# Optimization experiments

Measured on AMD Instinct MI355X. Metric: run time of the kernel, lower is better.

## Reference

```python
import jax, jax.numpy as jnp
import numpy as np

NUM_HEADS = 16


def setup_inputs() -> dict:
    key = jax.random.key(0)
    ks = jax.random.split(key, 5)
    B, S, D = 2, 2048, 2048
    scale = 1.0 / np.sqrt(D)
    return {
        "x": jax.random.normal(ks[0], (B, S, D), dtype=jnp.float32),
        "W_q": jax.random.normal(ks[1], (D, D), dtype=jnp.float32) * scale,
        "W_k": jax.random.normal(ks[2], (D, D), dtype=jnp.float32) * scale,
        "W_v": jax.random.normal(ks[3], (D, D), dtype=jnp.float32) * scale,
        "W_o": jax.random.normal(ks[4], (D, D), dtype=jnp.float32) * scale,
        "b_o": jnp.zeros((D,), dtype=jnp.float32),
    }


def reference(x, W_q, W_k, W_v, W_o, b_o):
    B, S, D = x.shape
    H = NUM_HEADS
    hd = D // H
    # projections, split into heads: [B, H, S, hd]
    q = (x @ W_q).reshape(B, S, H, hd).transpose(0, 2, 1, 3)
    k = (x @ W_k).reshape(B, S, H, hd).transpose(0, 2, 1, 3)
    v = (x @ W_v).reshape(B, S, H, hd).transpose(0, 2, 1, 3)
    # causal attention with explicit score matrix [B, H, S, S]
    scores = jnp.einsum("bhqd,bhkd->bhqk", q, k) / jnp.sqrt(jnp.asarray(hd, x.dtype))
    causal = jnp.tril(jnp.ones((S, S), dtype=bool))  # True = keep
    scores = jnp.where(causal, scores, -jnp.inf)
    weights = jax.nn.softmax(scores, axis=-1)
    ctx = jnp.einsum("bhqk,bhkd->bhqd", weights, v)
    ctx = ctx.transpose(0, 2, 1, 3).reshape(B, S, D)
    return ctx @ W_o + b_o
```

## Files before the change

kernel.cpp:

```cpp
#include <hip/hip_runtime.h>
#include <stdint.h>

#define SQ_S 2048
#define DIM 2048
#define NH 16
#define HD 128
#define NB 2
#define NROWS (NB * SQ_S)
#define NQK (2 * DIM)

typedef __bf16 bf16x8 __attribute__((ext_vector_type(8)));
typedef float f32x4 __attribute__((ext_vector_type(4)));
typedef unsigned short u16;

__device__ __forceinline__ u16 f2bf(float f) {
    unsigned int u = __float_as_uint(f);
    u += 0x7FFF + ((u >> 16) & 1);
    return (u16)(u >> 16);
}

__device__ __forceinline__ void load_lds16(const u16* g, u16* lds) {
    __builtin_amdgcn_global_load_lds(
        (const __attribute__((address_space(1))) unsigned int*)(uintptr_t)g,
        (__attribute__((address_space(3))) unsigned int*)(unsigned int)(uintptr_t)lds,
        16, 0, 0);
}

__global__ __launch_bounds__(256) void cast_x_kernel(const float* __restrict__ in,
                                                     u16* __restrict__ out) {
    int i = (blockIdx.x * 256 + threadIdx.x) * 4;
    float4 v = *(const float4*)(in + i);
    ushort4 o;
    o.x = f2bf(v.x); o.y = f2bf(v.y); o.z = f2bf(v.z); o.w = f2bf(v.w);
    *(ushort4*)(out + i) = o;
}

__global__ __launch_bounds__(256) void transpose_w_kernel(
    const float* __restrict__ w0, const float* __restrict__ w1,
    const float* __restrict__ w2, const float* __restrict__ w3,
    u16* __restrict__ o0, u16* __restrict__ o1,
    u16* __restrict__ o2, u16* __restrict__ o3) {
    __shared__ u16 tile[64][65];
    int z = blockIdx.z;
    const float* in = z == 0 ? w0 : z == 1 ? w1 : z == 2 ? w2 : w3;
    u16* out = z == 0 ? o0 : z == 1 ? o1 : z == 2 ? o2 : o3;
    int r0 = blockIdx.y * 64, c0 = blockIdx.x * 64;
    int t = threadIdx.x;
#pragma unroll
    for (int i = 0; i < 16; ++i) {
        int idx = i * 256 + t;
        int r = idx >> 6, c = idx & 63;
        tile[r][c] = f2bf(in[(size_t)(r0 + r) * DIM + c0 + c]);
    }
    __syncthreads();
#pragma unroll
    for (int i = 0; i < 4; ++i) {
        int idx = i * 256 + t;
        int oc = idx >> 4;
        int r4 = (idx & 15) * 4;
        ushort4 v;
        v.x = tile[r4 + 0][oc]; v.y = tile[r4 + 1][oc];
        v.z = tile[r4 + 2][oc]; v.w = tile[r4 + 3][oc];
        *(ushort4*)(out + (size_t)(c0 + oc) * DIM + r0 + r4) = v;
    }
}

__global__ __launch_bounds__(256) void gemm_bt_bf16(const u16* __restrict__ A,
                                                    const u16* __restrict__ Bt,
                                                    u16* __restrict__ C,
                                                    int M, int N, int K) {
    __shared__ u16 As[128 * 64];
    __shared__ u16 Bs[128 * 64];
    int t = threadIdx.x;
    int w = t >> 6, l = t & 63;
    int wm = (w >> 1) * 64, wn = (w & 1) * 64;
    int lr = l & 15, q = l >> 4;
    int bm = blockIdx.y, bn = blockIdx.x;
    int st_gcol = (((t & 7) ^ ((t >> 3) & 7)) * 8);
    f32x4 acc[4][4] = {};

    for (int k0 = 0; k0 < K; k0 += 64) {
        __syncthreads();
#pragma unroll
        for (int c = 0; c < 4; ++c) {
            int e = c * 2048 + t * 8;
            int row = e >> 6;
            load_lds16(A + (size_t)(bm * 128 + row) * K + k0 + st_gcol, As + e);
        }
#pragma unroll
        for (int c = 0; c < 4; ++c) {
            int e = c * 2048 + t * 8;
            int row = e >> 6;
            load_lds16(Bt + (size_t)(bn * 128 + row) * K + k0 + st_gcol, Bs + e);
        }
        __syncthreads();
#pragma unroll
        for (int kk = 0; kk < 2; ++kk) {
            bf16x8 a[4], b[4];
#pragma unroll
            for (int mt = 0; mt < 4; ++mt)
                a[mt] = *(const bf16x8*)(As + (wm + mt * 16 + lr) * 64 +
                                         (((kk * 4 + q) ^ (lr & 7)) * 8));
#pragma unroll
            for (int nt = 0; nt < 4; ++nt)
                b[nt] = *(const bf16x8*)(Bs + (wn + nt * 16 + lr) * 64 +
                                         (((kk * 4 + q) ^ (lr & 7)) * 8));
#pragma unroll
            for (int mt = 0; mt < 4; ++mt)
#pragma unroll
                for (int nt = 0; nt < 4; ++nt)
                    acc[mt][nt] = __builtin_amdgcn_mfma_f32_16x16x32_bf16(a[mt], b[nt], acc[mt][nt], 0, 0, 0);
        }
    }
    int r0 = bm * 128 + wm, c0 = bn * 128 + wn;
#pragma unroll
    for (int mt = 0; mt < 4; ++mt)
#pragma unroll
        for (int nt = 0; nt < 4; ++nt)
#pragma unroll
            for (int r = 0; r < 4; ++r) {
                int row = r0 + mt * 16 + q * 4 + r;
                int col = c0 + nt * 16 + lr;
                C[(size_t)row * N + col] = f2bf(acc[mt][nt][r]);
            }
}

__global__ __launch_bounds__(256) void gemm_bt_f32b(const u16* __restrict__ A,
                                                    const u16* __restrict__ Bt,
                                                    float* __restrict__ C,
                                                    const float* __restrict__ bias,
                                                    int M, int N, int K) {
    __shared__ u16 As[128 * 64];
    __shared__ u16 Bs[128 * 64];
    int t = threadIdx.x;
    int w = t >> 6, l = t & 63;
    int wm = (w >> 1) * 64, wn = (w & 1) * 64;
    int lr = l & 15, q = l >> 4;
    int bm = blockIdx.y, bn = blockIdx.x;
    int st_gcol = (((t & 7) ^ ((t >> 3) & 7)) * 8);
    f32x4 acc[4][4] = {};

    for (int k0 = 0; k0 < K; k0 += 64) {
        __syncthreads();
#pragma unroll
        for (int c = 0; c < 4; ++c) {
            int e = c * 2048 + t * 8;
            int row = e >> 6;
            load_lds16(A + (size_t)(bm * 128 + row) * K + k0 + st_gcol, As + e);
        }
#pragma unroll
        for (int c = 0; c < 4; ++c) {
            int e = c * 2048 + t * 8;
            int row = e >> 6;
            load_lds16(Bt + (size_t)(bn * 128 + row) * K + k0 + st_gcol, Bs + e);
        }
        __syncthreads();
#pragma unroll
        for (int kk = 0; kk < 2; ++kk) {
            bf16x8 a[4], b[4];
#pragma unroll
            for (int mt = 0; mt < 4; ++mt)
                a[mt] = *(const bf16x8*)(As + (wm + mt * 16 + lr) * 64 +
                                         (((kk * 4 + q) ^ (lr & 7)) * 8));
#pragma unroll
            for (int nt = 0; nt < 4; ++nt)
                b[nt] = *(const bf16x8*)(Bs + (wn + nt * 16 + lr) * 64 +
                                         (((kk * 4 + q) ^ (lr & 7)) * 8));
#pragma unroll
            for (int mt = 0; mt < 4; ++mt)
#pragma unroll
                for (int nt = 0; nt < 4; ++nt)
                    acc[mt][nt] = __builtin_amdgcn_mfma_f32_16x16x32_bf16(a[mt], b[nt], acc[mt][nt], 0, 0, 0);
        }
    }
    int r0 = bm * 128 + wm, c0 = bn * 128 + wn;
#pragma unroll
    for (int mt = 0; mt < 4; ++mt)
#pragma unroll
        for (int nt = 0; nt < 4; ++nt)
#pragma unroll
            for (int r = 0; r < 4; ++r) {
                int row = r0 + mt * 16 + q * 4 + r;
                int col = c0 + nt * 16 + lr;
                C[(size_t)row * N + col] = acc[mt][nt][r] + bias[col];
            }
}

__global__ __launch_bounds__(256) void attn_kernel(const u16* __restrict__ Q,
                                                   const u16* __restrict__ K,
                                                   const u16* __restrict__ Vt,
                                                   u16* __restrict__ ctx,
                                                   int ldqk, int ldv) {
    __shared__ u16 Kl[2][64 * 128];
    __shared__ u16 Vl[2][128 * 64];
    __shared__ u16 Pl[4][16 * 64];
    int t = threadIdx.x;
    int w = t >> 6, l = t & 63;
    int lr = l & 15, q = l >> 4, lk = q * 8;
    int px = blockIdx.x, h = blockIdx.y, b = blockIdx.z;
    const float scale = 0.08838834764831845f;
    int stK_gcol = (((t & 15) ^ (t >> 4)) * 8);
    int stV_gcol = (((t & 7) ^ ((t >> 3) & 7)) * 8);
    const u16* Kbase = K + (size_t)b * SQ_S * ldqk + h * HD;
    const u16* Vbase = Vt + (size_t)(h * HD) * ldv + b * SQ_S;

#pragma unroll 1
    for (int pass = 0; pass < 2; ++pass) {
        int qt = pass == 0 ? px : 31 - px;
        int q0 = qt * 64;
        int njt = qt + 1;

        bf16x8 qf[4];
        {
            const u16* qp = Q + ((size_t)(b * SQ_S + q0 + w * 16 + lr)) * ldqk + h * HD;
#pragma unroll
            for (int kd = 0; kd < 4; ++kd)
                qf[kd] = *(const bf16x8*)(qp + kd * 32 + lk);
        }

        f32x4 o[8] = {};
        float l_r[4] = {0.f, 0.f, 0.f, 0.f};

        {
            int e = t * 8;
#pragma unroll
            for (int c = 0; c < 4; ++c) {
                int eK = c * 2048 + e;
                load_lds16(Kbase + (size_t)(eK >> 7) * ldqk + stK_gcol, Kl[0] + eK);
            }
#pragma unroll
            for (int c = 0; c < 4; ++c) {
                int eV = c * 2048 + e;
                load_lds16(Vbase + (size_t)(eV >> 6) * ldv + stV_gcol, Vl[0] + eV);
            }
        }

#pragma unroll 1
        for (int jt = 0; jt < njt; ++jt) {
            __syncthreads();
            if (jt + 1 < njt) {
                int j1 = (jt + 1) * 64;
                u16* Kd = Kl[(jt + 1) & 1];
                u16* Vd = Vl[(jt + 1) & 1];
                int e = t * 8;
#pragma unroll
                for (int c = 0; c < 4; ++c) {
                    int eK = c * 2048 + e;
                    load_lds16(Kbase + (size_t)(j1 + (eK >> 7)) * ldqk + stK_gcol, Kd + eK);
                }
#pragma unroll
                for (int c = 0; c < 4; ++c) {
                    int eV = c * 2048 + e;
                    load_lds16(Vbase + (size_t)(eV >> 6) * ldv + j1 + stV_gcol, Vd + eV);
                }
            }
            const u16* Kc = Kl[jt & 1];
            const u16* Vc = Vl[jt & 1];

            f32x4 s[4] = {};
#pragma unroll
            for (int kd = 0; kd < 4; ++kd) {
#pragma unroll
                for (int nt = 0; nt < 4; ++nt) {
                    bf16x8 kb = *(const bf16x8*)(Kc + (nt * 16 + lr) * 128 +
                                                 (((kd * 4 + q) ^ lr) * 8));
                    s[nt] = __builtin_amdgcn_mfma_f32_16x16x32_bf16(qf[kd], kb, s[nt], 0, 0, 0);
                }
            }
            bool diag = (jt == qt);
            float rs[4] = {0.f, 0.f, 0.f, 0.f};
            float pv[4][4];
#pragma unroll
            for (int nt = 0; nt < 4; ++nt)
#pragma unroll
                for (int r = 0; r < 4; ++r) {
                    float v = s[nt][r] * scale - 6.0f;
                    if (diag && (nt * 16 + lr > w * 16 + q * 4 + r)) v = -1.0e30f;
                    float pp = __expf(v);
                    pv[nt][r] = pp;
                    rs[r] += pp;
                }
#pragma unroll
            for (int d = 1; d < 16; d <<= 1)
#pragma unroll
                for (int r = 0; r < 4; ++r)
                    rs[r] += __shfl_xor(rs[r], d, 64);
#pragma unroll
            for (int r = 0; r < 4; ++r)
                l_r[r] += rs[r];
            u16* pw = Pl[w];
#pragma unroll
            for (int nt = 0; nt < 4; ++nt)
#pragma unroll
                for (int r = 0; r < 4; ++r) {
                    int prow = q * 4 + r;
                    int pcol = nt * 16 + lr;
                    pw[prow * 64 + (((pcol >> 3) ^ (prow & 7)) * 8) + (pcol & 7)] = f2bf(pv[nt][r]);
                }
            asm volatile("s_waitcnt lgkmcnt(0)" ::: "memory");
#pragma unroll
            for (int kj = 0; kj < 2; ++kj) {
                bf16x8 pa = *(const bf16x8*)(pw + lr * 64 + (((kj * 4 + q) ^ (lr & 7)) * 8));
#pragma unroll
                for (int nd = 0; nd < 8; ++nd) {
                    bf16x8 vb = *(const bf16x8*)(Vc + (nd * 16 + lr) * 64 +
                                                 (((kj * 4 + q) ^ (lr & 7)) * 8));
                    o[nd] = __builtin_amdgcn_mfma_f32_16x16x32_bf16(pa, vb, o[nd], 0, 0, 0);
                }
            }
        }
        float li[4];
#pragma unroll
        for (int r = 0; r < 4; ++r) li[r] = 1.f / l_r[r];
#pragma unroll
        for (int nd = 0; nd < 8; ++nd)
#pragma unroll
            for (int r = 0; r < 4; ++r) {
                int row = q0 + w * 16 + q * 4 + r;
                int col = h * HD + nd * 16 + lr;
                ctx[((size_t)(b * SQ_S + row)) * DIM + col] = f2bf(o[nd][r] * li[r]);
            }
        __syncthreads();
    }
}

extern "C" void kernel_launch(void* const* d_in, const int* in_sizes, int n_in,
                              void* d_out, int out_size, void* d_ws, size_t ws_size,
                              hipStream_t stream) {
    const float* x  = (const float*)d_in[0];
    const float* Wq = (const float*)d_in[1];
    const float* Wk = (const float*)d_in[2];
    const float* Wv = (const float*)d_in[3];
    const float* Wo = (const float*)d_in[4];
    const float* bo = (const float*)d_in[5];
    float* out = (float*)d_out;

    char* p = (char*)d_ws;
    const size_t SZ_ACT = (size_t)NROWS * DIM * 2;
    const size_t SZ_W   = (size_t)DIM * DIM * 2;
    u16* Xb   = (u16*)(p);
    u16* Wqkt = (u16*)(p + SZ_ACT);
    u16* Wvt  = (u16*)(p + SZ_ACT + 2 * SZ_W);
    u16* Wot  = (u16*)(p + SZ_ACT + 3 * SZ_W);
    u16* QK   = (u16*)(p + SZ_ACT + 4 * SZ_W);
    u16* Vt   = (u16*)(p + 3 * SZ_ACT + 4 * SZ_W);
    u16* Cx   = (u16*)(p + 4 * SZ_ACT + 4 * SZ_W);

    cast_x_kernel<<<(NROWS * DIM) / 1024, 256, 0, stream>>>(x, Xb);
    transpose_w_kernel<<<dim3(DIM / 64, DIM / 64, 4), 256, 0, stream>>>(
        Wq, Wk, Wv, Wo,
        Wqkt, Wqkt + (size_t)DIM * DIM, Wvt, Wot);
    gemm_bt_bf16<<<dim3(NQK / 128, NROWS / 128), 256, 0, stream>>>(Xb, Wqkt, QK, NROWS, NQK, DIM);
    gemm_bt_bf16<<<dim3(NROWS / 128, DIM / 128), 256, 0, stream>>>(Wvt, Xb, Vt, DIM, NROWS, DIM);
    attn_kernel<<<dim3(16, NH, NB), 256, 0, stream>>>(QK, QK + DIM, Vt, Cx, NQK, NROWS);
    gemm_bt_f32b<<<dim3(DIM / 128, NROWS / 128), 256, 0, stream>>>(Cx, Wot, out, bo, NROWS, DIM, DIM);
}
```

Before: 410.1 us.

## Fuse QKV projection, read K/V from global in attention, split-K output GEMM

```diff
diff --git a/kernel.cpp b/kernel.cpp
--- a/kernel.cpp
+++ b/kernel.cpp
@@ -7,7 +7,7 @@
 #define HD 128
 #define NB 2
 #define NROWS (NB * SQ_S)
-#define NQK (2 * DIM)
+#define NQKV (3 * DIM)
 
 typedef __bf16 bf16x8 __attribute__((ext_vector_type(8)));
 typedef float f32x4 __attribute__((ext_vector_type(4)));
@@ -65,6 +65,28 @@
     }
 }
 
+__global__ __launch_bounds__(256) void transpose_v_kernel(const u16* __restrict__ V,
+                                                          u16* __restrict__ Vt, int ldv) {
+    __shared__ u16 tile[64][72];
+    int s0 = blockIdx.x * 64, d0 = blockIdx.y * 64;
+    int bh = blockIdx.z;
+    int b = bh >> 4, h = bh & 15;
+    int t = threadIdx.x;
+#pragma unroll
+    for (int i = 0; i < 16; ++i) {
+        int idx = i * 256 + t;
+        int r = idx >> 6, c = idx & 63;
+        tile[r][c] = V[((size_t)(b * SQ_S + s0 + r)) * ldv + h * HD + d0 + c];
+    }
+    __syncthreads();
+#pragma unroll
+    for (int i = 0; i < 16; ++i) {
+        int idx = i * 256 + t;
+        int r = idx >> 6, c = idx & 63;
+        Vt[((size_t)(bh * HD + d0 + r)) * SQ_S + s0 + c] = tile[c][r];
+    }
+}
+
 __global__ __launch_bounds__(256) void gemm_bt_bf16(const u16* __restrict__ A,
                                                     const u16* __restrict__ Bt,
                                                     u16* __restrict__ C,
@@ -125,22 +147,23 @@
             }
 }
 
-__global__ __launch_bounds__(256) void gemm_bt_f32b(const u16* __restrict__ A,
+__global__ __launch_bounds__(256) void gemm_bt_f32s(const u16* __restrict__ A,
                                                     const u16* __restrict__ Bt,
-                                                    float* __restrict__ C,
-                                                    const float* __restrict__ bias,
-                                                    int M, int N, int K) {
+                                                    float* __restrict__ Cpart,
+                                                    int M, int N, int K, int Khalf) {
     __shared__ u16 As[128 * 64];
     __shared__ u16 Bs[128 * 64];
     int t = threadIdx.x;
     int w = t >> 6, l = t & 63;
     int wm = (w >> 1) * 64, wn = (w & 1) * 64;
     int lr = l & 15, q = l >> 4;
-    int bm = blockIdx.y, bn = blockIdx.x;
+    int bm = blockIdx.y, bn = blockIdx.x, z = blockIdx.z;
     int st_gcol = (((t & 7) ^ ((t >> 3) & 7)) * 8);
     f32x4 acc[4][4] = {};
-
-    for (int k0 = 0; k0 < K; k0 += 64) {
+    int kbeg = z * Khalf;
+
+    for (int kk0 = 0; kk0 < Khalf; kk0 += 64) {
+        int k0 = kbeg + kk0;
         __syncthreads();
 #pragma unroll
         for (int c = 0; c < 4; ++c) {
@@ -173,6 +196,7 @@
                     acc[mt][nt] = __builtin_amdgcn_mfma_f32_16x16x32_bf16(a[mt], b[nt], acc[mt][nt], 0, 0, 0);
         }
     }
+    float* Cp = Cpart + (size_t)z * M * N;
     int r0 = bm * 128 + wm, c0 = bn * 128 + wn;
 #pragma unroll
     for (int mt = 0; mt < 4; ++mt)
@@ -182,33 +206,42 @@
             for (int r = 0; r < 4; ++r) {
                 int row = r0 + mt * 16 + q * 4 + r;
                 int col = c0 + nt * 16 + lr;
-                C[(size_t)row * N + col] = acc[mt][nt][r] + bias[col];
-            }
+                Cp[(size_t)row * N + col] = acc[mt][nt][r];
+            }
+}
+
+__global__ __launch_bounds__(256) void reduce_bias_kernel(const float* __restrict__ P,
+                                                          float* __restrict__ out,
+                                                          const float* __restrict__ bias) {
+    int i = (blockIdx.x * 256 + threadIdx.x) * 4;
+    const size_t MN = (size_t)NROWS * DIM;
+    float4 a = *(const float4*)(P + i);
+    float4 c = *(const float4*)(P + MN + i);
+    float4 bb = *(const float4*)(bias + (i & (DIM - 1)));
+    float4 o;
+    o.x = a.x + c.x + bb.x; o.y = a.y + c.y + bb.y;
+    o.z = a.z + c.z + bb.z; o.w = a.w + c.w + bb.w;
+    *(float4*)(out + i) = o;
 }
 
 __global__ __launch_bounds__(256) void attn_kernel(const u16* __restrict__ Q,
                                                    const u16* __restrict__ K,
                                                    const u16* __restrict__ Vt,
-                                                   u16* __restrict__ ctx,
-                                                   int ldqk, int ldv) {
-    __shared__ u16 Kl[2][64 * 128];
-    __shared__ u16 Vl[2][128 * 64];
+                                                   u16* __restrict__ ctx, int ldqk) {
     __shared__ u16 Pl[4][16 * 64];
     int t = threadIdx.x;
     int w = t >> 6, l = t & 63;
     int lr = l & 15, q = l >> 4, lk = q * 8;
     int px = blockIdx.x, h = blockIdx.y, b = blockIdx.z;
     const float scale = 0.08838834764831845f;
-    int stK_gcol = (((t & 15) ^ (t >> 4)) * 8);
-    int stV_gcol = (((t & 7) ^ ((t >> 3) & 7)) * 8);
     const u16* Kbase = K + (size_t)b * SQ_S * ldqk + h * HD;
-    const u16* Vbase = Vt + (size_t)(h * HD) * ldv + b * SQ_S;
+    const u16* Vbase = Vt + ((size_t)(b * NH + h)) * HD * SQ_S;
+    u16* pw = Pl[w];
 
 #pragma unroll 1
     for (int pass = 0; pass < 2; ++pass) {
         int qt = pass == 0 ? px : 31 - px;
         int q0 = qt * 64;
-        int njt = qt + 1;
 
         bf16x8 qf[4];
         {
@@ -221,49 +254,16 @@
         f32x4 o[8] = {};
         float l_r[4] = {0.f, 0.f, 0.f, 0.f};
 
-        {
-            int e = t * 8;
-#pragma unroll
-            for (int c = 0; c < 4; ++c) {
-                int eK = c * 2048 + e;
-                load_lds16(Kbase + (size_t)(eK >> 7) * ldqk + stK_gcol, Kl[0] + eK);
-            }
-#pragma unroll
-            for (int c = 0; c < 4; ++c) {
-                int eV = c * 2048 + e;
-                load_lds16(Vbase + (size_t)(eV >> 6) * ldv + stV_gcol, Vl[0] + eV);
-            }
-        }
-
 #pragma unroll 1
-        for (int jt = 0; jt < njt; ++jt) {
-            __syncthreads();
-            if (jt + 1 < njt) {
-                int j1 = (jt + 1) * 64;
-                u16* Kd = Kl[(jt + 1) & 1];
-                u16* Vd = Vl[(jt + 1) & 1];
-                int e = t * 8;
-#pragma unroll
-                for (int c = 0; c < 4; ++c) {
-                    int eK = c * 2048 + e;
-                    load_lds16(Kbase + (size_t)(j1 + (eK >> 7)) * ldqk + stK_gcol, Kd + eK);
-                }
-#pragma unroll
-                for (int c = 0; c < 4; ++c) {
-                    int eV = c * 2048 + e;
-                    load_lds16(Vbase + (size_t)(eV >> 6) * ldv + j1 + stV_gcol, Vd + eV);
-                }
-            }
-            const u16* Kc = Kl[jt & 1];
-            const u16* Vc = Vl[jt & 1];
-
+        for (int jt = 0; jt <= qt; ++jt) {
+            int j0 = jt * 64;
             f32x4 s[4] = {};
 #pragma unroll
             for (int kd = 0; kd < 4; ++kd) {
 #pragma unroll
                 for (int nt = 0; nt < 4; ++nt) {
-                    bf16x8 kb = *(const bf16x8*)(Kc + (nt * 16 + lr) * 128 +
-                                                 (((kd * 4 + q) ^ lr) * 8));
+                    bf16x8 kb = *(const bf16x8*)(Kbase + (size_t)(j0 + nt * 16 + lr) * ldqk +
+                                                 kd * 32 + lk);
                     s[nt] = __builtin_amdgcn_mfma_f32_16x16x32_bf16(qf[kd], kb, s[nt], 0, 0, 0);
                 }
             }
@@ -288,7 +288,6 @@
 #pragma unroll
             for (int r = 0; r < 4; ++r)
                 l_r[r] += rs[r];
-            u16* pw = Pl[w];
 #pragma unroll
             for (int nt = 0; nt < 4; ++nt)
 #pragma unroll
@@ -303,8 +302,8 @@
                 bf16x8 pa = *(const bf16x8*)(pw + lr * 64 + (((kj * 4 + q) ^ (lr & 7)) * 8));
 #pragma unroll
                 for (int nd = 0; nd < 8; ++nd) {
-                    bf16x8 vb = *(const bf16x8*)(Vc + (nd * 16 + lr) * 64 +
-                                                 (((kj * 4 + q) ^ (lr & 7)) * 8));
+                    bf16x8 vb = *(const bf16x8*)(Vbase + (size_t)(nd * 16 + lr) * SQ_S +
+                                                 j0 + kj * 32 + lk);
                     o[nd] = __builtin_amdgcn_mfma_f32_16x16x32_bf16(pa, vb, o[nd], 0, 0, 0);
                 }
             }
@@ -320,7 +319,6 @@
                 int col = h * HD + nd * 16 + lr;
                 ctx[((size_t)(b * SQ_S + row)) * DIM + col] = f2bf(o[nd][r] * li[r]);
             }
-        __syncthreads();
     }
 }
 
@@ -336,22 +334,24 @@
     float* out = (float*)d_out;
 
     char* p = (char*)d_ws;
-    const size_t SZ_ACT = (size_t)NROWS * DIM * 2;
-    const size_t SZ_W   = (size_t)DIM * DIM * 2;
-    u16* Xb   = (u16*)(p);
-    u16* Wqkt = (u16*)(p + SZ_ACT);
-    u16* Wvt  = (u16*)(p + SZ_ACT + 2 * SZ_W);
-    u16* Wot  = (u16*)(p + SZ_ACT + 3 * SZ_W);
-    u16* QK   = (u16*)(p + SZ_ACT + 4 * SZ_W);
-    u16* Vt   = (u16*)(p + 3 * SZ_ACT + 4 * SZ_W);
-    u16* Cx   = (u16*)(p + 4 * SZ_ACT + 4 * SZ_W);
+    const size_t SZ_ACT  = (size_t)NROWS * DIM * 2;
+    const size_t SZ_W    = (size_t)DIM * DIM * 2;
+    const size_t SZ_QKV  = (size_t)NROWS * NQKV * 2;
+    u16*   Xb   = (u16*)(p);
+    u16*   Wqkv = (u16*)(p + SZ_ACT);
+    u16*   Wot  = (u16*)(p + SZ_ACT + 3 * SZ_W);
+    u16*   QKV  = (u16*)(p + SZ_ACT + 4 * SZ_W);
+    u16*   Vt   = (u16*)(p + SZ_ACT + 4 * SZ_W + SZ_QKV);
+    u16*   Cx   = (u16*)(p + 2 * SZ_ACT + 4 * SZ_W + SZ_QKV);
+    float* Pp   = (float*)(p + SZ_ACT + 4 * SZ_W);
 
     cast_x_kernel<<<(NROWS * DIM) / 1024, 256, 0, stream>>>(x, Xb);
     transpose_w_kernel<<<dim3(DIM / 64, DIM / 64, 4), 256, 0, stream>>>(
         Wq, Wk, Wv, Wo,
-        Wqkt, Wqkt + (size_t)DIM * DIM, Wvt, Wot);
-    gemm_bt_bf16<<<dim3(NQK / 128, NROWS / 128), 256, 0, stream>>>(Xb, Wqkt, QK, NROWS, NQK, DIM);
-    gemm_bt_bf16<<<dim3(NROWS / 128, DIM / 128), 256, 0, stream>>>(Wvt, Xb, Vt, DIM, NROWS, DIM);
-    attn_kernel<<<dim3(16, NH, NB), 256, 0, stream>>>(QK, QK + DIM, Vt, Cx, NQK, NROWS);
-    gemm_bt_f32b<<<dim3(DIM / 128, NROWS / 128), 256, 0, stream>>>(Cx, Wot, out, bo, NROWS, DIM, DIM);
-}
+        Wqkv, Wqkv + (size_t)DIM * DIM, Wqkv + 2 * (size_t)DIM * DIM, Wot);
+    gemm_bt_bf16<<<dim3(NQKV / 128, NROWS / 128), 256, 0, stream>>>(Xb, Wqkv, QKV, NROWS, NQKV, DIM);
+    transpose_v_kernel<<<dim3(SQ_S / 64, HD / 64, NB * NH), 256, 0, stream>>>(QKV + 2 * DIM, Vt, NQKV);
+    attn_kernel<<<dim3(16, NH, NB), 256, 0, stream>>>(QKV, QKV + DIM, Vt, Cx, NQKV);
+    gemm_bt_f32s<<<dim3(DIM / 128, NROWS / 128, 2), 256, 0, stream>>>(Cx, Wot, Pp, NROWS, DIM, DIM, DIM / 2);
+    reduce_bias_kernel<<<(NROWS * DIM) / 1024, 256, 0, stream>>>(Pp, out, bo);
+}
```

Result: slower. 630.0 us (+53.6%).
